# Optimization experiments

Measured on AMD Instinct MI355X. Metric: run time of the kernel, lower is better.

Reference implementation:

```python
import jax, jax.numpy as jnp
import numpy as np

DIM = 128
HIDDEN = 512
T_END = 1.0
N_STEPS = 32  # fixed-step RK4 in place of adaptive dopri5


def setup_inputs() -> dict:
    key = jax.random.key(0)
    ks = jax.random.split(key, 8)
    d, h = DIM, HIDDEN
    x = jax.random.normal(ks[0], (65536, d), dtype=jnp.float32)
    # Rademacher probe vector for the Hutchinson trace estimator (fixed per forward pass)
    v = jnp.sign(jax.random.normal(ks[1], (65536, d), dtype=jnp.float32))
    v = jnp.where(v == 0, 1.0, v)
    # ODEF: MLP on concat([z, t]) -> hidden -> hidden -> dim, tanh activations
    s1 = 1.0 / np.sqrt(d + 1)
    s2 = 1.0 / np.sqrt(h)
    W1 = jax.random.uniform(ks[2], (d + 1, h), jnp.float32, -s1, s1)
    b1 = jnp.zeros((h,), jnp.float32)
    W2 = jax.random.uniform(ks[3], (h, h), jnp.float32, -s2, s2)
    b2 = jnp.zeros((h,), jnp.float32)
    W3 = jax.random.uniform(ks[4], (h, d), jnp.float32, -s2, s2)
    b3 = jnp.zeros((d,), jnp.float32)
    return {"x": x, "v": v, "W1": W1, "b1": b1, "W2": W2, "b2": b2, "W3": W3, "b3": b3}


def _mlp(t, z, W1, b1, W2, b2, W3, b3):
    # z: [B, D], t: scalar -> f(z, t): [B, D]
    tt = jnp.full((z.shape[0], 1), t, dtype=z.dtype)
    h = jnp.tanh(jnp.concatenate([z, tt], axis=1) @ W1 + b1)
    h = jnp.tanh(h @ W2 + b2)
    return h @ W3 + b3


def _dynamics(t, z, v, params):
    # returns dz/dt = f and dlogp/dt = -Tr(df/dz) ~= -(v^T J) . v
    f, vjp_fn = jax.vjp(lambda zz: _mlp(t, zz, *params), z)
    (vJ,) = vjp_fn(v)
    div = jnp.sum(vJ * v, axis=1)  # [B]
    return f, -div


def _integrate(x, v, params):
    dt = T_END / N_STEPS
    logp0 = jnp.zeros((x.shape[0],), x.dtype)

    def rk4_step(carry, i):
        z, lp = carry
        t = i.astype(x.dtype) * dt
        k1f, k1d = _dynamics(t, z, v, params)
        k2f, k2d = _dynamics(t + 0.5 * dt, z + 0.5 * dt * k1f, v, params)
        k3f, k3d = _dynamics(t + 0.5 * dt, z + 0.5 * dt * k2f, v, params)
        k4f, k4d = _dynamics(t + dt, z + dt * k3f, v, params)
        z_new = z + (dt / 6.0) * (k1f + 2.0 * k2f + 2.0 * k3f + k4f)
        lp_new = lp + (dt / 6.0) * (k1d + 2.0 * k2d + 2.0 * k3d + k4d)
        return (z_new, lp_new), None

    (zT, logpT), _ = jax.lax.scan(rk4_step, (x, logp0), jnp.arange(N_STEPS))
    return zT, logpT


def reference(x, v, W1, b1, W2, b2, W3, b3):
    params = (W1, b1, W2, b2, W3, b3)
    zT, logpT = _integrate(x, v, params)
    d = x.shape[1]
    log2pi = jnp.asarray(np.log(2.0 * np.pi), x.dtype)
    prior_lp = -0.5 * jnp.sum(zT * zT, axis=1) - 0.5 * d * log2pi  # N(0, I) log-density
    return prior_lp + logpT  # [B] log p(x)
```

## Files before the change

### kernel.cpp

```cpp
#include <hip/hip_runtime.h>


#define DIMV 128
#define HIDV 512
#define ROWS 64
#define PAN_STR 536
#define ZS_STR  136

typedef float  floatx4 __attribute__((ext_vector_type(4)));
typedef short  short8  __attribute__((ext_vector_type(8)));
typedef unsigned int uint4v __attribute__((ext_vector_type(4)));

static __device__ __forceinline__ unsigned short f2bf(float x) {
    union { float f; unsigned int u; } c; c.f = x;
    unsigned int u = c.u;
    u += 0x7FFFu + ((u >> 16) & 1u);
    return (unsigned short)(u >> 16);
}
static __device__ __forceinline__ float bf2f(unsigned short h) {
    union { unsigned int u; float f; } c; c.u = ((unsigned int)h) << 16;
    return c.f;
}
static __device__ __forceinline__ float fast_tanh(float x) {
    x = fminf(8.0f, fmaxf(-8.0f, x));
    float e = exp2f(x * 2.8853900817779268f);
    return (e - 1.0f) * __builtin_amdgcn_rcpf(e + 1.0f);
}

__global__ void pack_kernel(const float* __restrict__ src, unsigned short* __restrict__ dst,
                            int K, int N, int ld, int transpose) {
    int i = blockIdx.x * 256 + threadIdx.x;
    if (i >= K * N) return;
    int j  = i & 7;
    int n  = (i >> 3) % N;
    int k8 = (i >> 3) / N;
    int k  = k8 * 8 + j;
    float v = transpose ? src[n * ld + k] : src[k * ld + n];
    dst[i] = f2bf(v);
}

__global__ __launch_bounds__(256, 2) void vg_k(const float* __restrict__ v,
                                               const unsigned short* __restrict__ Wp,
                                               unsigned short* __restrict__ out0) {
    __shared__ __align__(16) unsigned short As[128 * 72];
    const int tid  = threadIdx.x;
    const int wave = tid >> 6, lane = tid & 63;
    const int quad = lane >> 4, l16 = lane & 15;
    const int row0 = blockIdx.x * 128;
    const int colw = blockIdx.y * 256 + wave * 64;

    floatx4 acc[8][4];
    #pragma unroll
    for (int m = 0; m < 8; ++m)
        #pragma unroll
        for (int f = 0; f < 4; ++f) { floatx4 zz = {0.f,0.f,0.f,0.f}; acc[m][f] = zz; }

    for (int k0 = 0; k0 < 128; k0 += 64) {
        __syncthreads();
        {
            const int r  = tid >> 3;
            const int cc = (tid & 7) << 3;
            #pragma unroll
            for (int i = 0; i < 4; ++i) {
                const int rr = r + (i << 5);
                const size_t base = (size_t)(row0 + rr) * 128 + k0 + cc;
                float vals[8];
                *(float4*)&vals[0] = *(const float4*)&v[base];
                *(float4*)&vals[4] = *(const float4*)&v[base + 4];
                short8 sv;
                #pragma unroll
                for (int j = 0; j < 8; ++j) sv[j] = (short)f2bf(vals[j]);
                *reinterpret_cast<short8*>(&As[rr * 72 + cc]) = sv;
            }
        }
        __syncthreads();
        #pragma unroll
        for (int kt = 0; kt < 2; ++kt) {
            const int k8 = (k0 >> 3) + (kt << 2) + quad;
            short8 b[4];
            #pragma unroll
            for (int f = 0; f < 4; ++f)
                b[f] = *reinterpret_cast<const short8*>(
                    &Wp[((size_t)k8 * 512 + colw + (f << 4) + l16) << 3]);
            #pragma unroll
            for (int m = 0; m < 8; ++m) {
                const short8 a = *reinterpret_cast<const short8*>(
                    &As[(m * 16 + l16) * 72 + (kt << 5) + (quad << 3)]);
                #pragma unroll
                for (int f = 0; f < 4; ++f)
                    acc[m][f] = __builtin_amdgcn_mfma_f32_16x16x32_bf16(a, b[f], acc[m][f], 0, 0, 0);
            }
        }
    }
    #pragma unroll
    for (int m = 0; m < 8; ++m)
        #pragma unroll
        for (int f = 0; f < 4; ++f) {
            const int col = colw + (f << 4) + l16;
            #pragma unroll
            for (int r = 0; r < 4; ++r) {
                const int row = row0 + m * 16 + quad * 4 + r;
                out0[(size_t)row * 512 + col] = f2bf(acc[m][f][r]);
            }
        }
}

struct OArgs {
    const float* x;
    const unsigned short* W1zp;
    const unsigned short* W2p;
    const unsigned short* W3p;
    const unsigned short* W2Tp;
    const unsigned short* g3;
    const unsigned short* u;
    const float* b1;
    const float* w1t;
    const float* b2;
    const float* b3;
    float* z;
    float* lp;
};

__global__ __launch_bounds__(1024, 4) void ode_k(OArgs p) {
    __shared__ __align__(16) unsigned short H1s[ROWS * PAN_STR];
    __shared__ __align__(16) unsigned short Hss[ROWS * PAN_STR];
    __shared__ __align__(16) unsigned short Zss[ROWS * ZS_STR];
    const int tid  = threadIdx.x;
    const int wave = tid >> 6, lane = tid & 63;
    const int quad = lane >> 4, l16 = lane & 15;
    const int row0 = blockIdx.x * ROWS;
    const int colw = wave << 5;
    const int sr = tid >> 4;
    const int sc = (tid & 15) << 3;
    const size_t gbase = (size_t)(row0 + sr) * 512;
    const int colB = ((wave & 7) << 4) + l16;
    const int rowB = (wave >> 3) << 5;

    short8 g3v[4];
    #pragma unroll
    for (int j = 0; j < 4; ++j)
        g3v[j] = *reinterpret_cast<const short8*>(&p.g3[gbase + sc + (j << 7)]);
    float b1v[2], w1tv[2], b2v[2];
    #pragma unroll
    for (int f = 0; f < 2; ++f) {
        const int col = colw + (f << 4) + l16;
        b1v[f] = p.b1[col]; w1tv[f] = p.w1t[col]; b2v[f] = p.b2[col];
    }
    const float b3v = p.b3[colB];

    float z_r[2][4];
    #pragma unroll
    for (int m = 0; m < 2; ++m)
        #pragma unroll
        for (int r = 0; r < 4; ++r) {
            const int row = rowB + m * 16 + quad * 4 + r;
            const float val = p.x[(size_t)(row0 + row) * 128 + colB];
            z_r[m][r] = val;
            Zss[row * ZS_STR + colB] = f2bf(val);
        }
    float accf_r[2][4];
    float accd_r = 0.0f, lp_r = 0.0f;

    const float dt = 1.0f / 32.0f;
    floatx4 acc[4][2];

    for (int e = 0; e < 128; ++e) {
        const int s = e & 3;
        const int step = e >> 2;
        const bool s0 = (s == 0), s3 = (s == 3);
        const float tph  = (s == 0) ? 0.0f : (s == 3 ? dt : 0.5f * dt);
        const float t    = (float)step * dt + tph;
        const float wrk  = (s == 1 || s == 2) ? (dt / 3.0f) : (dt / 6.0f);
        const float cnext = (s <= 1) ? 0.5f * dt : (s == 2 ? dt : 0.0f);

        __syncthreads();

        #pragma unroll
        for (int m = 0; m < 4; ++m)
            #pragma unroll
            for (int f = 0; f < 2; ++f) { floatx4 zz = {0.f,0.f,0.f,0.f}; acc[m][f] = zz; }
        #pragma unroll
        for (int kt = 0; kt < 4; ++kt) {
            const int k8 = (kt << 2) + quad;
            short8 b[2];
            #pragma unroll
            for (int f = 0; f < 2; ++f)
                b[f] = *reinterpret_cast<const short8*>(
                    &p.W1zp[((size_t)k8 * 512 + colw + (f << 4) + l16) << 3]);
            #pragma unroll
            for (int m = 0; m < 4; ++m) {
                const short8 a = *reinterpret_cast<const short8*>(
                    &Zss[(m * 16 + l16) * ZS_STR + (kt << 5) + (quad << 3)]);
                #pragma unroll
                for (int f = 0; f < 2; ++f)
                    acc[m][f] = __builtin_amdgcn_mfma_f32_16x16x32_bf16(a, b[f], acc[m][f], 0, 0, 0);
            }
        }
        #pragma unroll
        for (int m = 0; m < 4; ++m)
            #pragma unroll
            for (int f = 0; f < 2; ++f) {
                const int col = colw + (f << 4) + l16;
                const float bias = b1v[f] + t * w1tv[f];
                #pragma unroll
                for (int r = 0; r < 4; ++r) {
                    const int row = m * 16 + quad * 4 + r;
                    H1s[row * PAN_STR + col] = f2bf(fast_tanh(acc[m][f][r] + bias));
                }
            }
        __syncthreads();

        #pragma unroll
        for (int m = 0; m < 4; ++m)
            #pragma unroll
            for (int f = 0; f < 2; ++f) { floatx4 zz = {0.f,0.f,0.f,0.f}; acc[m][f] = zz; }
        #pragma unroll 4
        for (int kt = 0; kt < 16; ++kt) {
            const int k8 = (kt << 2) + quad;
            short8 b[2];
            #pragma unroll
            for (int f = 0; f < 2; ++f)
                b[f] = *reinterpret_cast<const short8*>(
                    &p.W2p[((size_t)k8 * 512 + colw + (f << 4) + l16) << 3]);
            #pragma unroll
            for (int m = 0; m < 4; ++m) {
                const short8 a = *reinterpret_cast<const short8*>(
                    &H1s[(m * 16 + l16) * PAN_STR + (kt << 5) + (quad << 3)]);
                #pragma unroll
                for (int f = 0; f < 2; ++f)
                    acc[m][f] = __builtin_amdgcn_mfma_f32_16x16x32_bf16(a, b[f], acc[m][f], 0, 0, 0);
            }
        }
        #pragma unroll
        for (int m = 0; m < 4; ++m)
            #pragma unroll
            for (int f = 0; f < 2; ++f) {
                const int col = colw + (f << 4) + l16;
                #pragma unroll
                for (int r = 0; r < 4; ++r) {
                    const int row = m * 16 + quad * 4 + r;
                    Hss[row * PAN_STR + col] = f2bf(fast_tanh(acc[m][f][r] + b2v[f]));
                }
            }
        __syncthreads();

        {
            floatx4 accb[2];
            #pragma unroll
            for (int m = 0; m < 2; ++m) { floatx4 zz = {0.f,0.f,0.f,0.f}; accb[m] = zz; }
            #pragma unroll 4
            for (int kt = 0; kt < 16; ++kt) {
                const int k8 = (kt << 2) + quad;
                const short8 b = *reinterpret_cast<const short8*>(
                    &p.W3p[((size_t)k8 * 128 + colB) << 3]);
                #pragma unroll
                for (int m = 0; m < 2; ++m) {
                    const short8 a = *reinterpret_cast<const short8*>(
                        &Hss[(rowB + m * 16 + l16) * PAN_STR + (kt << 5) + (quad << 3)]);
                    accb[m] = __builtin_amdgcn_mfma_f32_16x16x32_bf16(a, b, accb[m], 0, 0, 0);
                }
            }
            #pragma unroll
            for (int m = 0; m < 2; ++m) {
                #pragma unroll
                for (int r = 0; r < 4; ++r) {
                    const int row = rowB + m * 16 + quad * 4 + r;
                    const float x = accb[m][r] + b3v;
                    const float a = wrk * x + (s0 ? 0.0f : accf_r[m][r]);
                    if (s3) {
                        z_r[m][r] += a;
                        Zss[row * ZS_STR + colB] = f2bf(z_r[m][r]);
                    } else {
                        accf_r[m][r] = a;
                        Zss[row * ZS_STR + colB] = f2bf(z_r[m][r] + cnext * x);
                    }
                }
            }
        }
        __syncthreads();

        #pragma unroll
        for (int j = 0; j < 4; ++j) {
            const int cc = sc + (j << 7);
            const short8 hv = *reinterpret_cast<const short8*>(&Hss[sr * PAN_STR + cc]);
            short8 ov;
            #pragma unroll
            for (int el = 0; el < 8; ++el) {
                const float h = bf2f((unsigned short)hv[el]);
                const float g = bf2f((unsigned short)g3v[j][el]);
                const float gh = g * h;
                ov[el] = (short)f2bf(fmaf(-gh, h, g));
            }
            *reinterpret_cast<short8*>(&Hss[sr * PAN_STR + cc]) = ov;
        }
        __syncthreads();

        #pragma unroll
        for (int m = 0; m < 4; ++m)
            #pragma unroll
            for (int f = 0; f < 2; ++f) { floatx4 zz = {0.f,0.f,0.f,0.f}; acc[m][f] = zz; }
        #pragma unroll 4
        for (int kt = 0; kt < 16; ++kt) {
            const int k8 = (kt << 2) + quad;
            short8 b[2];
            #pragma unroll
            for (int f = 0; f < 2; ++f)
                b[f] = *reinterpret_cast<const short8*>(
                    &p.W2Tp[((size_t)k8 * 512 + colw + (f << 4) + l16) << 3]);
            #pragma unroll
            for (int m = 0; m < 4; ++m) {
                const short8 a = *reinterpret_cast<const short8*>(
                    &Hss[(m * 16 + l16) * PAN_STR + (kt << 5) + (quad << 3)]);
                #pragma unroll
                for (int f = 0; f < 2; ++f)
                    acc[m][f] = __builtin_amdgcn_mfma_f32_16x16x32_bf16(a, b[f], acc[m][f], 0, 0, 0);
            }
        }
        __syncthreads();
        #pragma unroll
        for (int m = 0; m < 4; ++m)
            #pragma unroll
            for (int f = 0; f < 2; ++f) {
                const int col = colw + (f << 4) + l16;
                #pragma unroll
                for (int r = 0; r < 4; ++r) {
                    const int row = m * 16 + quad * 4 + r;
                    Hss[row * PAN_STR + col] = f2bf(acc[m][f][r]);
                }
            }
        __syncthreads();

        {
            float sum = 0.0f;
            #pragma unroll
            for (int j = 0; j < 4; ++j) {
                const int cc = sc + (j << 7);
                const short8 xv = *reinterpret_cast<const short8*>(&Hss[sr * PAN_STR + cc]);
                const short8 hv = *reinterpret_cast<const short8*>(&H1s[sr * PAN_STR + cc]);
                const short8 uv = *reinterpret_cast<const short8*>(&p.u[gbase + cc]);
                #pragma unroll
                for (int el = 0; el < 8; ++el) {
                    const float x = bf2f((unsigned short)xv[el]);
                    const float h = bf2f((unsigned short)hv[el]);
                    const float uu = bf2f((unsigned short)uv[el]);
                    sum += x * (1.0f - h * h) * uu;
                }
            }
            sum += __shfl_xor(sum, 1);
            sum += __shfl_xor(sum, 2);
            sum += __shfl_xor(sum, 4);
            sum += __shfl_xor(sum, 8);
            const float a = wrk * (-sum) + (s0 ? 0.0f : accd_r);
            if (s3) lp_r += a;
            else    accd_r = a;
        }
    }

    #pragma unroll
    for (int m = 0; m < 2; ++m)
        #pragma unroll
        for (int r = 0; r < 4; ++r)
            p.z[(size_t)(row0 + rowB + m * 16 + quad * 4 + r) * 128 + colB] = z_r[m][r];
    if ((tid & 15) == 0) p.lp[row0 + sr] = lp_r;
}

__global__ void final_k(const float* __restrict__ z, const float* __restrict__ lp,
                        float* __restrict__ out) {
    const int tid = threadIdx.x;
    const int row = blockIdx.x * 16 + (tid >> 4);
    const int l16 = tid & 15;
    const float4* zr = (const float4*)&z[(size_t)row * 128 + (l16 << 3)];
    float4 a = zr[0], b = zr[1];
    float s = a.x*a.x + a.y*a.y + a.z*a.z + a.w*a.w
            + b.x*b.x + b.y*b.y + b.z*b.z + b.w*b.w;
    s += __shfl_xor(s, 1);
    s += __shfl_xor(s, 2);
    s += __shfl_xor(s, 4);
    s += __shfl_xor(s, 8);
    if (l16 == 0) out[row] = lp[row] - 0.5f * s - 117.6241322501981f;
}

extern "C" void kernel_launch(void* const* d_in, const int* in_sizes, int n_in,
                              void* d_out, int out_size, void* d_ws, size_t ws_size,
                              hipStream_t stream) {
    (void)n_in; (void)out_size;
    const float* x  = (const float*)d_in[0];
    const float* v  = (const float*)d_in[1];
    const float* W1 = (const float*)d_in[2];
    const float* b1 = (const float*)d_in[3];
    const float* W2 = (const float*)d_in[4];
    const float* b2 = (const float*)d_in[5];
    const float* W3 = (const float*)d_in[6];
    const float* b3 = (const float*)d_in[7];
    float* out = (float*)d_out;
    const int B = in_sizes[0] / DIMV;

    auto al = [](size_t s) { return (s + 255) & ~(size_t)255; };
    auto need_for = [&](size_t C) {
        size_t s = 0;
        s += al(C * DIMV * 4);
        s += al(C * 4);
        s += al(C * HIDV * 2) * 2;
        s += al(128 * 512 * 2) * 3 + al(512 * 512 * 2) * 2;
        return s;
    };
    size_t C = 32768;
    while (C > 1024 && need_for(C) > ws_size) C >>= 1;
    if (need_for(C) > ws_size) return;

    char* w = (char*)d_ws;
    auto alloc = [&](size_t bytes) { char* p = w; w += al(bytes); return p; };
    float* z    = (float*)alloc(C * DIMV * 4);
    float* lp   = (float*)alloc(C * 4);
    unsigned short* g3 = (unsigned short*)alloc(C * HIDV * 2);
    unsigned short* u  = (unsigned short*)alloc(C * HIDV * 2);
    unsigned short* W1zp  = (unsigned short*)alloc(128 * 512 * 2);
    unsigned short* W3p   = (unsigned short*)alloc(512 * 128 * 2);
    unsigned short* W3Tp  = (unsigned short*)alloc(128 * 512 * 2);
    unsigned short* W2p   = (unsigned short*)alloc(512 * 512 * 2);
    unsigned short* W2Tp  = (unsigned short*)alloc(512 * 512 * 2);

    auto pack = [&](const float* src, unsigned short* dst, int K, int N, int ld, int tr) {
        pack_kernel<<<dim3((K * N + 255) / 256), dim3(256), 0, stream>>>(src, dst, K, N, ld, tr);
    };
    pack(W1, W1zp,  128, 512, 512, 0);
    pack(W2, W2p,   512, 512, 512, 0);
    pack(W3, W3p,   512, 128, 128, 0);
    pack(W2, W2Tp,  512, 512, 512, 1);
    pack(W1, W3Tp,  512, 128, 512, 1);
    pack(W3, W3Tp,  128, 512, 128, 1);

    const int GM128 = (int)C / 128;
    const int GMF   = (int)C / ROWS;

    for (int c0 = 0; c0 < B; c0 += (int)C) {
        const float* xc = x + (size_t)c0 * DIMV;
        const float* vc = v + (size_t)c0 * DIMV;

        vg_k<<<dim3(GM128, 2), 256, 0, stream>>>(vc, W3Tp, g3);
        vg_k<<<dim3(GM128, 2), 256, 0, stream>>>(vc, W1zp, u);

        OArgs q{};
        q.x = xc;
        q.W1zp = W1zp; q.W2p = W2p; q.W3p = W3p; q.W2Tp = W2Tp;
        q.g3 = g3; q.u = u;
        q.b1 = b1; q.w1t = W1 + 128 * 512; q.b2 = b2; q.b3 = b3;
        q.z = z; q.lp = lp;
        ode_k<<<dim3(GMF), 1024, 0, stream>>>(q);

        final_k<<<dim3((int)C / 16), 256, 0, stream>>>(z, lp, out + c0);
    }
}
```

Baseline: 19.86 ms.

## Fuse tanh-derivative factors into GEMM epilogues and reduce divergence from registers

Each thread now keeps the per-row g3 and u probe values in registers in MFMA fragment layout. The tanh-derivative scaling is folded into the layer-1 and layer-2 epilogues, so the separate elementwise passes over shared memory and their extra barriers go away. The backward GEMM result is no longer written to LDS; it is multiplied by the stored factors and reduced with shuffles plus a small shared buffer. The chunk size now covers the whole batch, and a redundant pack launch is dropped. The cost is higher register pressure at 1024 threads per block and a reordered barrier pattern.

After: 27.47 ms. +38.3%, slower.

```diff
diff --git a/kernel.cpp b/kernel.cpp
--- a/kernel.cpp
+++ b/kernel.cpp
@@ -9,7 +9,6 @@
 
 typedef float  floatx4 __attribute__((ext_vector_type(4)));
 typedef short  short8  __attribute__((ext_vector_type(8)));
-typedef unsigned int uint4v __attribute__((ext_vector_type(4)));
 
 static __device__ __forceinline__ unsigned short f2bf(float x) {
     union { float f; unsigned int u; } c; c.f = x;
@@ -125,21 +124,30 @@
     __shared__ __align__(16) unsigned short H1s[ROWS * PAN_STR];
     __shared__ __align__(16) unsigned short Hss[ROWS * PAN_STR];
     __shared__ __align__(16) unsigned short Zss[ROWS * ZS_STR];
+    __shared__ float div_s[ROWS * 17];
     const int tid  = threadIdx.x;
     const int wave = tid >> 6, lane = tid & 63;
     const int quad = lane >> 4, l16 = lane & 15;
     const int row0 = blockIdx.x * ROWS;
     const int colw = wave << 5;
-    const int sr = tid >> 4;
-    const int sc = (tid & 15) << 3;
-    const size_t gbase = (size_t)(row0 + sr) * 512;
     const int colB = ((wave & 7) << 4) + l16;
     const int rowB = (wave >> 3) << 5;
 
-    short8 g3v[4];
-    #pragma unroll
-    for (int j = 0; j < 4; ++j)
-        g3v[j] = *reinterpret_cast<const short8*>(&p.g3[gbase + sc + (j << 7)]);
+    unsigned int g3p[4][2][2], up[4][2][2];
+    #pragma unroll
+    for (int m = 0; m < 4; ++m)
+        #pragma unroll
+        for (int f = 0; f < 2; ++f) {
+            const int col = colw + (f << 4) + l16;
+            #pragma unroll
+            for (int pr = 0; pr < 2; ++pr) {
+                const int row = row0 + m * 16 + quad * 4 + pr * 2;
+                g3p[m][f][pr] = (unsigned int)p.g3[(size_t)row * 512 + col]
+                              | ((unsigned int)p.g3[(size_t)(row + 1) * 512 + col] << 16);
+                up[m][f][pr]  = (unsigned int)p.u[(size_t)row * 512 + col]
+                              | ((unsigned int)p.u[(size_t)(row + 1) * 512 + col] << 16);
+            }
+        }
     float b1v[2], w1tv[2], b2v[2];
     #pragma unroll
     for (int f = 0; f < 2; ++f) {
@@ -163,6 +171,8 @@
 
     const float dt = 1.0f / 32.0f;
     floatx4 acc[4][2];
+    unsigned int facp[4][2][2];
+    __syncthreads();
 
     for (int e = 0; e < 128; ++e) {
         const int s = e & 3;
@@ -173,8 +183,6 @@
         const float wrk  = (s == 1 || s == 2) ? (dt / 3.0f) : (dt / 6.0f);
         const float cnext = (s <= 1) ? 0.5f * dt : (s == 2 ? dt : 0.0f);
 
-        __syncthreads();
-
         #pragma unroll
         for (int m = 0; m < 4; ++m)
             #pragma unroll
@@ -202,11 +210,19 @@
             for (int f = 0; f < 2; ++f) {
                 const int col = colw + (f << 4) + l16;
                 const float bias = b1v[f] + t * w1tv[f];
+                unsigned int fp0 = 0, fp1 = 0;
                 #pragma unroll
                 for (int r = 0; r < 4; ++r) {
                     const int row = m * 16 + quad * 4 + r;
-                    H1s[row * PAN_STR + col] = f2bf(fast_tanh(acc[m][f][r] + bias));
+                    const unsigned short hb = f2bf(fast_tanh(acc[m][f][r] + bias));
+                    H1s[row * PAN_STR + col] = hb;
+                    const float thr = bf2f(hb);
+                    const float uu  = bf2f((unsigned short)(up[m][f][r >> 1] >> ((r & 1) << 4)));
+                    const float fac = fmaf(-thr * thr, uu, uu);
+                    const unsigned int fb = (unsigned int)f2bf(fac) << ((r & 1) << 4);
+                    if (r < 2) fp0 |= fb; else fp1 |= fb;
                 }
+                facp[m][f][0] = fp0; facp[m][f][1] = fp1;
             }
         __syncthreads();
 
@@ -231,6 +247,8 @@
                     acc[m][f] = __builtin_amdgcn_mfma_f32_16x16x32_bf16(a, b[f], acc[m][f], 0, 0, 0);
             }
         }
+        __syncthreads();
+
         #pragma unroll
         for (int m = 0; m < 4; ++m)
             #pragma unroll
@@ -239,7 +257,12 @@
                 #pragma unroll
                 for (int r = 0; r < 4; ++r) {
                     const int row = m * 16 + quad * 4 + r;
-                    Hss[row * PAN_STR + col] = f2bf(fast_tanh(acc[m][f][r] + b2v[f]));
+                    const unsigned short h2b = f2bf(fast_tanh(acc[m][f][r] + b2v[f]));
+                    Hss[row * PAN_STR + col] = h2b;
+                    const float h2r = bf2f(h2b);
+                    const float g3f = bf2f((unsigned short)(g3p[m][f][r >> 1] >> ((r & 1) << 4)));
+                    const float gh  = g3f * h2r;
+                    H1s[row * PAN_STR + col] = f2bf(fmaf(-gh, h2r, g3f));
                 }
             }
         __syncthreads();
@@ -277,23 +300,6 @@
                 }
             }
         }
-        __syncthreads();
-
-        #pragma unroll
-        for (int j = 0; j < 4; ++j) {
-            const int cc = sc + (j << 7);
-            const short8 hv = *reinterpret_cast<const short8*>(&Hss[sr * PAN_STR + cc]);
-            short8 ov;
-            #pragma unroll
-            for (int el = 0; el < 8; ++el) {
-                const float h = bf2f((unsigned short)hv[el]);
-                const float g = bf2f((unsigned short)g3v[j][el]);
-                const float gh = g * h;
-                ov[el] = (short)f2bf(fmaf(-gh, h, g));
-            }
-            *reinterpret_cast<short8*>(&Hss[sr * PAN_STR + cc]) = ov;
-        }
-        __syncthreads();
 
         #pragma unroll
         for (int m = 0; m < 4; ++m)
@@ -310,47 +316,33 @@
             #pragma unroll
             for (int m = 0; m < 4; ++m) {
                 const short8 a = *reinterpret_cast<const short8*>(
-                    &Hss[(m * 16 + l16) * PAN_STR + (kt << 5) + (quad << 3)]);
+                    &H1s[(m * 16 + l16) * PAN_STR + (kt << 5) + (quad << 3)]);
                 #pragma unroll
                 for (int f = 0; f < 2; ++f)
                     acc[m][f] = __builtin_amdgcn_mfma_f32_16x16x32_bf16(a, b[f], acc[m][f], 0, 0, 0);
             }
         }
-        __syncthreads();
-        #pragma unroll
-        for (int m = 0; m < 4; ++m)
-            #pragma unroll
-            for (int f = 0; f < 2; ++f) {
-                const int col = colw + (f << 4) + l16;
-                #pragma unroll
-                for (int r = 0; r < 4; ++r) {
-                    const int row = m * 16 + quad * 4 + r;
-                    Hss[row * PAN_STR + col] = f2bf(acc[m][f][r]);
-                }
+        #pragma unroll
+        for (int m = 0; m < 4; ++m)
+            #pragma unroll
+            for (int r = 0; r < 4; ++r) {
+                float pdv = acc[m][0][r] * bf2f((unsigned short)(facp[m][0][r >> 1] >> ((r & 1) << 4)))
+                          + acc[m][1][r] * bf2f((unsigned short)(facp[m][1][r >> 1] >> ((r & 1) << 4)));
+                pdv += __shfl_xor(pdv, 1);
+                pdv += __shfl_xor(pdv, 2);
+                pdv += __shfl_xor(pdv, 4);
+                pdv += __shfl_xor(pdv, 8);
+                if (l16 == 0) div_s[(m * 16 + quad * 4 + r) * 17 + wave] = pdv;
             }
         __syncthreads();
 
         {
-            float sum = 0.0f;
-            #pragma unroll
-            for (int j = 0; j < 4; ++j) {
-                const int cc = sc + (j << 7);
-                const short8 xv = *reinterpret_cast<const short8*>(&Hss[sr * PAN_STR + cc]);
-                const short8 hv = *reinterpret_cast<const short8*>(&H1s[sr * PAN_STR + cc]);
-                const short8 uv = *reinterpret_cast<const short8*>(&p.u[gbase + cc]);
-                #pragma unroll
-                for (int el = 0; el < 8; ++el) {
-                    const float x = bf2f((unsigned short)xv[el]);
-                    const float h = bf2f((unsigned short)hv[el]);
-                    const float uu = bf2f((unsigned short)uv[el]);
-                    sum += x * (1.0f - h * h) * uu;
-                }
-            }
-            sum += __shfl_xor(sum, 1);
-            sum += __shfl_xor(sum, 2);
-            sum += __shfl_xor(sum, 4);
-            sum += __shfl_xor(sum, 8);
-            const float a = wrk * (-sum) + (s0 ? 0.0f : accd_r);
+            float part = div_s[(tid >> 4) * 17 + (tid & 15)];
+            part += __shfl_xor(part, 1);
+            part += __shfl_xor(part, 2);
+            part += __shfl_xor(part, 4);
+            part += __shfl_xor(part, 8);
+            const float a = wrk * (-part) + (s0 ? 0.0f : accd_r);
             if (s3) lp_r += a;
             else    accd_r = a;
         }
@@ -361,7 +353,7 @@
         #pragma unroll
         for (int r = 0; r < 4; ++r)
             p.z[(size_t)(row0 + rowB + m * 16 + quad * 4 + r) * 128 + colB] = z_r[m][r];
-    if ((tid & 15) == 0) p.lp[row0 + sr] = lp_r;
+    if ((tid & 15) == 0) p.lp[row0 + (tid >> 4)] = lp_r;
 }
 
 __global__ void final_k(const float* __restrict__ z, const float* __restrict__ lp,
@@ -404,9 +396,10 @@
         s += al(128 * 512 * 2) * 3 + al(512 * 512 * 2) * 2;
         return s;
     };
-    size_t C = 32768;
+    size_t C = 65536;
     while (C > 1024 && need_for(C) > ws_size) C >>= 1;
     if (need_for(C) > ws_size) return;
+    if (C > (size_t)B) C = B;
 
     char* w = (char*)d_ws;
     auto alloc = [&](size_t bytes) { char* p = w; w += al(bytes); return p; };
@@ -427,7 +420,6 @@
     pack(W2, W2p,   512, 512, 512, 0);
     pack(W3, W3p,   512, 128, 128, 0);
     pack(W2, W2Tp,  512, 512, 512, 1);
-    pack(W1, W3Tp,  512, 128, 512, 1);
     pack(W3, W3Tp,  128, 512, 128, 1);
 
     const int GM128 = (int)C / 128;
```
